# Kernel tuning notes

Measured on AMD Instinct MI355X. Metric: run time of the kernel, lower is better.

Reference implementation:

```python
import jax, jax.numpy as jnp
import numpy as np

N_NODES_PER_GRAPH = 200
N_GRAPHS = 32
N = N_NODES_PER_GRAPH * N_GRAPHS        # 6400 nodes
E = N_GRAPHS * N_NODES_PER_GRAPH ** 2   # 1.28M edges
IN_DIM = 200
HID = 32
HEADS = 1
N_CLASSES = 2
BN_EPS = 1e-5


def setup_inputs() -> dict:
    key = jax.random.key(0)
    ks = jax.random.split(key, 32)
    p = lambda k, shape: (jax.random.normal(k, shape, dtype=jnp.float32) * 0.1)
    inp = {
        'x': jax.random.normal(ks[0], (N, IN_DIM), dtype=jnp.float32),
        'edge_attr': jax.random.normal(ks[1], (E,), dtype=jnp.float32),
        'edge_index': jax.random.randint(ks[2], (2, E), 0, N),
        'batch': jax.random.randint(ks[3], (N,), 0, N_GRAPHS),
        # ---- GAT block 1 (in=200 -> hid=32) ----
        'w1': p(ks[4], (IN_DIM, HEADS * HID)),
        'asrc1': p(ks[5], (HEADS, HID)),
        'adst1': p(ks[6], (HEADS, HID)),
        'b1': p(ks[7], (HEADS * HID,)),
        'elw1': p(ks[8], (2 * HID + 1, HID)),   # edge_lin for edge_node_concate
        'elb1': p(ks[9], (HID,)),
        'pw1': p(ks[10], (HEADS * HID, HID)),   # block projection Linear
        'pb1': p(ks[11], (HID,)),
        'bng1': 1.0 + p(ks[12], (HID,)),
        'bnb1': p(ks[13], (HID,)),
        # ---- GAT block 2 (in=32 -> hid=32, proj=final_node_dim=32) ----
        'w2': p(ks[14], (HID, HEADS * HID)),
        'asrc2': p(ks[15], (HEADS, HID)),
        'adst2': p(ks[16], (HEADS, HID)),
        'b2': p(ks[17], (HEADS * HID,)),
        'elw2': p(ks[18], (2 * HID + 1, HID)),
        'elb2': p(ks[19], (HID,)),
        'pw2': p(ks[20], (HEADS * HID, HID)),
        'pb2': p(ks[21], (HID,)),
        'bng2': 1.0 + p(ks[22], (HID,)),
        'bnb2': p(ks[23], (HID,)),
        # ---- classifier head (BasicMLP as single Linear) ----
        'fw': p(ks[24], (HID, N_CLASSES)),
        'fb': p(ks[25], (N_CLASSES,)),
    }
    return inp


def _gat_block(x, src, dst, ew_abs, W, asrc, adst, b, elw, elb, pw, pb, bng, bnb):
    """MPGATConv(edge_node_concate) + Linear + LeakyReLU + BatchNorm1d(eval)."""
    n = x.shape[0]
    H, C = asrc.shape
    xp = (x @ W).reshape(n, H, C)                       # [N,H,C] per-head projection
    al_s = jnp.sum(xp * asrc, axis=-1)                  # [N,H] alpha_src
    al_d = jnp.sum(xp * adst, axis=-1)                  # [N,H] alpha_dst
    a = jax.nn.leaky_relu(al_s[src] + al_d[dst], 0.2)   # [E,H]
    # scatter-softmax over destination index
    m = jax.ops.segment_max(a, dst, num_segments=n)
    m = jnp.where(jnp.isfinite(m), m, 0.0)
    e = jnp.exp(a - m[dst])
    s = jax.ops.segment_sum(e, dst, num_segments=n)
    alpha = e / jnp.where(s[dst] == 0, 1.0, s[dst])     # [E,H]
    # message: concat(x_i, x_j * alpha, |edge_w|) -> edge_lin
    ewb = jnp.broadcast_to(ew_abs[:, None, None], (ew_abs.shape[0], H, 1))
    msg = jnp.concatenate([xp[dst], xp[src] * alpha[..., None], ewb], axis=-1)
    msg = msg @ elw + elb                               # [E,H,C]
    agg = jax.ops.segment_sum(msg, dst, num_segments=n).reshape(n, H * C) + b
    # block tail: Linear -> LeakyReLU -> BatchNorm1d (eval, running stats 0/1)
    z = jax.nn.leaky_relu(agg @ pw + pb, 0.2)
    z = z * (bng / np.float32(np.sqrt(1.0 + BN_EPS))) + bnb
    return z


def reference(x, edge_attr,
              w1, asrc1, adst1, b1, elw1, elb1, pw1, pb1, bng1, bnb1,
              w2, asrc2, adst2, b2, elw2, elb2, pw2, pb2, bng2, bnb2,
              fw, fb, edge_index, batch):
    src, dst = edge_index[0], edge_index[1]             # j (source), i (target)
    ew = jnp.abs(edge_attr)                             # use_abs_weight=True
    z = _gat_block(x, src, dst, ew, w1, asrc1, adst1, b1, elw1, elb1, pw1, pb1, bng1, bnb1)
    z = _gat_block(z, src, dst, ew, w2, asrc2, adst2, b2, elw2, elb2, pw2, pb2, bng2, bnb2)
    # global mean pool over graphs
    tot = jax.ops.segment_sum(z, batch, num_segments=N_GRAPHS)
    cnt = jax.ops.segment_sum(jnp.ones((z.shape[0],), z.dtype), batch, num_segments=N_GRAPHS)
    g = tot / jnp.maximum(cnt, 1.0)[:, None]            # [B, HID]
    return g @ fw + fb                                  # [B, n_classes]
```

## Files before the change

kernel.cpp:

```cpp
#include <hip/hip_runtime.h>
#include <hip/hip_bf16.h>


#define HID 32
#define NB_SORT 512
#define BUCK_SHIFT 5
#define BUCK_BINS 32
#define NBUCK_MAX 256
#define ECAP 8192
#define DCAP 512

typedef unsigned short ushort_t;
typedef unsigned int uint_t;

__device__ __forceinline__ ushort_t f2bf(float f) {
    uint_t u = __float_as_uint(f);
    u += 0x7FFF + ((u >> 16) & 1);
    return (ushort_t)(u >> 16);
}
__device__ __forceinline__ float bf2f(ushort_t h) {
    return __uint_as_float(((uint_t)h) << 16);
}

__global__ void k_bhist(const int* __restrict__ dst, int* __restrict__ bpart_T,
                        int E, int nbuck, int nb, int chunk) {
    __shared__ int h[NBUCK_MAX];
    for (int i = threadIdx.x; i < nbuck; i += blockDim.x) h[i] = 0;
    __syncthreads();
    int b = blockIdx.x;
    int lo = b * chunk, hi = min(lo + chunk, E);
    for (int e = lo + threadIdx.x; e < hi; e += blockDim.x)
        atomicAdd(&h[dst[e] >> BUCK_SHIFT], 1);
    __syncthreads();
    for (int g = threadIdx.x; g < nbuck; g += blockDim.x)
        bpart_T[(size_t)g * nb + b] = h[g];
}

__global__ void k_bcur(const int* __restrict__ bpart_T, int* __restrict__ bcur_T,
                       int* __restrict__ bcnt, float* __restrict__ pool,
                       int nb, int poolN) {
    __shared__ int wsum_[4];
    int g = blockIdx.x;
    if (g == 0)
        for (int i = threadIdx.x; i < poolN; i += blockDim.x) pool[i] = 0.f;
    const int2* row = (const int2*)(bpart_T + (size_t)g * nb);
    int t = threadIdx.x;
    int2 v = row[t];
    int s = v.x + v.y;
    int lane = t & 63, wid = t >> 6;
    int p = s;
    #pragma unroll
    for (int d = 1; d < 64; d <<= 1) { int u = __shfl_up(p, d); if (lane >= d) p += u; }
    if (lane == 63) wsum_[wid] = p;
    __syncthreads();
    int add = 0;
    for (int i = 0; i < wid; i++) add += wsum_[i];
    int excl = p + add - s;
    int2 w; w.x = excl; w.y = excl + v.x;
    ((int2*)(bcur_T + (size_t)g * nb))[t] = w;
    if (t == blockDim.x - 1) bcnt[g] = excl + s;
}

__global__ void k_bscatter(const int* __restrict__ src, const int* __restrict__ dst,
                           const float* __restrict__ ea, const int* __restrict__ bcur_T,
                           uint2* __restrict__ ebuf, int E, int nbuck, int nb, int chunk) {
    __shared__ int cur[NBUCK_MAX];
    int b = blockIdx.x;
    for (int g = threadIdx.x; g < nbuck; g += blockDim.x)
        cur[g] = (g << 13) + bcur_T[(size_t)g * nb + b];
    __syncthreads();
    int lo = b * chunk, hi = min(lo + chunk, E);
    for (int e = lo + threadIdx.x; e < hi; e += blockDim.x) {
        int d = dst[e];
        int p = atomicAdd(&cur[d >> BUCK_SHIFT], 1);
        uint2 v;
        v.x = ((uint_t)d << 16) | (uint_t)src[e];
        v.y = __float_as_uint(fabsf(ea[e]));
        ebuf[p] = v;
    }
}

__global__ void k_bsort(const uint2* __restrict__ ebuf, const int* __restrict__ bcnt,
                        int* __restrict__ begs, int* __restrict__ ends,
                        float* __restrict__ wsum, ushort_t* __restrict__ ssrc,
                        int nbins, int nbuck) {
    __shared__ int hist[BUCK_BINS];
    __shared__ int cur[BUCK_BINS];
    __shared__ int sexc[BUCK_BINS];
    __shared__ float hw[BUCK_BINS];
    __shared__ ushort_t sbuf[ECAP];
    int g = blockIdx.x;
    if (g >= nbuck) return;
    int binlo = g << BUCK_SHIFT;
    int nbin = min(BUCK_BINS, nbins - binlo);
    int base = g << 13;
    int cnt = bcnt[g];
    int t = threadIdx.x;
    if (t < BUCK_BINS) { hist[t] = 0; hw[t] = 0.f; }
    __syncthreads();
    for (int i = t; i < cnt; i += blockDim.x) {
        uint2 v = ebuf[base + i];
        int dl = (int)(v.x >> 16) - binlo;
        atomicAdd(&hist[dl], 1);
        atomicAdd(&hw[dl], __uint_as_float(v.y));
    }
    __syncthreads();
    if (t < BUCK_BINS) {
        int v = hist[t];
        int p = v;
        #pragma unroll
        for (int d = 1; d < 32; d <<= 1) { int u = __shfl_up(p, d); if (t >= d) p += u; }
        cur[t] = p - v;
        sexc[t] = p - v;
    }
    __syncthreads();
    if (t < nbin) {
        begs[binlo + t] = base + sexc[t];
        ends[binlo + t] = base + sexc[t] + hist[t];
        wsum[binlo + t] = hw[t];
    }
    if (cnt <= ECAP) {
        for (int i = t; i < cnt; i += blockDim.x) {
            uint_t v = ebuf[base + i].x;
            int dl = (int)(v >> 16) - binlo;
            int p = atomicAdd(&cur[dl], 1);
            sbuf[p] = (ushort_t)(v & 0xFFFFu);
        }
        __syncthreads();
        for (int i = t; i < cnt; i += blockDim.x)
            ssrc[base + i] = sbuf[i];
    } else {
        for (int i = t; i < cnt; i += blockDim.x) {
            uint_t v = ebuf[base + i].x;
            int dl = (int)(v >> 16) - binlo;
            int p = atomicAdd(&cur[dl], 1);
            ssrc[base + p] = (ushort_t)(v & 0xFFFFu);
        }
    }
}

__device__ __forceinline__ void node_epilogue(float xp, int r, int l,
        const float* __restrict__ asrc, const float* __restrict__ adst,
        const float* __restrict__ elw,
        ushort_t* __restrict__ ys, float* __restrict__ yd,
        float* __restrict__ als, float* __restrict__ ald) {
    float ps = xp * asrc[l], pd = xp * adst[l];
    #pragma unroll
    for (int mask = 16; mask >= 1; mask >>= 1) {
        ps += __shfl_xor(ps, mask);
        pd += __shfl_xor(pd, mask);
    }
    if (l == 0) { als[r] = ps; ald[r] = pd; }
    int gbase = threadIdx.x & 32;
    float yss = 0.f, ydd = 0.f;
    #pragma unroll
    for (int k = 0; k < HID; k++) {
        float xk = __shfl(xp, gbase + k);
        yss = fmaf(xk, elw[(HID + k) * HID + l], yss);
        ydd = fmaf(xk, elw[k * HID + l], ydd);
    }
    ys[r * HID + l] = f2bf(yss);
    yd[r * HID + l] = ydd;
}

__global__ void k_b1prep(const float* __restrict__ x, const float* __restrict__ w1,
                         const float* __restrict__ asrc, const float* __restrict__ adst,
                         const float* __restrict__ elw,
                         ushort_t* __restrict__ ys, float* __restrict__ yd,
                         float* __restrict__ als, float* __restrict__ ald,
                         int n, int K) {
    extern __shared__ float wlds[];
    for (int i = threadIdx.x; i < K * HID; i += blockDim.x) wlds[i] = w1[i];
    __syncthreads();
    int l = threadIdx.x & 31;
    int r = blockIdx.x * (blockDim.x >> 5) + (threadIdx.x >> 5);
    if (r >= n) return;
    const float4* rowv = (const float4*)(x + (size_t)r * K);
    float acc = 0.f;
    for (int k4 = 0; k4 < (K >> 2); k4++) {
        float4 v = rowv[k4];
        int k = k4 << 2;
        acc = fmaf(v.x, wlds[(k + 0) * HID + l], acc);
        acc = fmaf(v.y, wlds[(k + 1) * HID + l], acc);
        acc = fmaf(v.z, wlds[(k + 2) * HID + l], acc);
        acc = fmaf(v.w, wlds[(k + 3) * HID + l], acc);
    }
    node_epilogue(acc, r, l, asrc, adst, elw, ys, yd, als, ald);
}

#define LEAKY(a) ((a) >= 0.f ? (a) : 0.2f * (a))

__device__ __forceinline__ float gat_node_z(int node, int lane,
        float2* __restrict__ pbuf,
        const int* __restrict__ begs, const int* __restrict__ ends,
        const ushort_t* __restrict__ ssrc, const float* __restrict__ wsum,
        const float* __restrict__ als, const float* __restrict__ ald,
        const ushort_t* __restrict__ ys, const float* __restrict__ yd,
        const float* __restrict__ elw, const float* __restrict__ elb,
        const float* __restrict__ bvec, const float* __restrict__ pw,
        const float* __restrict__ pb, const float* __restrict__ bng,
        const float* __restrict__ bnb) {
    int beg = begs[node], end = ends[node];
    int deg = end - beg;
    int half = lane >> 5, l = lane & 31;
    float aldi = ald[node];
    float agg;
    if (deg > 0) {
        int degc = min(deg, DCAP);
        float mreg = -INFINITY;
        for (int i = lane; i < deg; i += 64) {
            int j = ssrc[beg + i];
            float a = LEAKY(als[j] + aldi);
            mreg = fmaxf(mreg, a);
            if (i < DCAP) { float2 p; p.x = a; p.y = __int_as_float(j); pbuf[i] = p; }
        }
        #pragma unroll
        for (int mask = 32; mask >= 1; mask >>= 1)
            mreg = fmaxf(mreg, __shfl_xor(mreg, mask));
        float m = mreg;
        __threadfence_block();
        float es = 0.f;
        for (int i = lane; i < degc; i += 64) {
            float w = __expf(pbuf[i].x - m);
            es += w;
            pbuf[i].x = w;
        }
        #pragma unroll
        for (int mask = 32; mask >= 1; mask >>= 1)
            es += __shfl_xor(es, mask);
        __threadfence_block();
        int mid = degc >> 1;
        int e = half ? mid : 0;
        int e1 = half ? degc : mid;
        float acc0 = 0.f, acc1 = 0.f;
        for (; e + 8 <= e1; e += 8) {
            float2 p0 = pbuf[e + 0], p1 = pbuf[e + 1], p2 = pbuf[e + 2], p3 = pbuf[e + 3];
            float2 p4 = pbuf[e + 4], p5 = pbuf[e + 5], p6 = pbuf[e + 6], p7 = pbuf[e + 7];
            acc0 = fmaf(p0.x, bf2f(ys[__float_as_int(p0.y) * HID + l]), acc0);
            acc1 = fmaf(p1.x, bf2f(ys[__float_as_int(p1.y) * HID + l]), acc1);
            acc0 = fmaf(p2.x, bf2f(ys[__float_as_int(p2.y) * HID + l]), acc0);
            acc1 = fmaf(p3.x, bf2f(ys[__float_as_int(p3.y) * HID + l]), acc1);
            acc0 = fmaf(p4.x, bf2f(ys[__float_as_int(p4.y) * HID + l]), acc0);
            acc1 = fmaf(p5.x, bf2f(ys[__float_as_int(p5.y) * HID + l]), acc1);
            acc0 = fmaf(p6.x, bf2f(ys[__float_as_int(p6.y) * HID + l]), acc0);
            acc1 = fmaf(p7.x, bf2f(ys[__float_as_int(p7.y) * HID + l]), acc1);
        }
        for (; e < e1; e++) {
            float2 p = pbuf[e];
            acc0 = fmaf(p.x, bf2f(ys[__float_as_int(p.y) * HID + l]), acc0);
        }
        float esT = 0.f;
        for (int e2 = beg + DCAP + half; e2 < end; e2 += 2) {
            int j = ssrc[e2];
            float w = __expf(LEAKY(als[j] + aldi) - m);
            esT += w;
            acc0 = fmaf(w, bf2f(ys[j * HID + l]), acc0);
        }
        float acc = acc0 + acc1;
        acc += __shfl_xor(acc, 32);
        esT += __shfl_xor(esT, 32);
        agg = acc / (es + esT) + wsum[node] * elw[64 * HID + l];
    } else {
        agg = 0.f;
    }
    agg += (float)deg * (yd[node * HID + l] + elb[l]) + bvec[l];
    float z = 0.f;
    #pragma unroll
    for (int k = 0; k < HID; k++) {
        float av = __shfl(agg, k);
        z = fmaf(av, pw[k * HID + l], z);
    }
    z += pb[l];
    z = LEAKY(z);
    const float inv = 0.99999500003749971875f;
    return fmaf(z, bng[l] * inv, bnb[l]);
}

__global__ void __launch_bounds__(256)
k_gat1(const int* __restrict__ begs, const int* __restrict__ ends,
       const ushort_t* __restrict__ ssrc, const float* __restrict__ wsum,
       const float* __restrict__ als, const float* __restrict__ ald,
       const ushort_t* __restrict__ ys, const float* __restrict__ yd,
       const float* __restrict__ elw, const float* __restrict__ elb,
       const float* __restrict__ bvec, const float* __restrict__ pw,
       const float* __restrict__ pb, const float* __restrict__ bng,
       const float* __restrict__ bnb,
       const float* __restrict__ w2, const float* __restrict__ asrc2,
       const float* __restrict__ adst2, const float* __restrict__ elw2,
       ushort_t* __restrict__ ys2, float* __restrict__ yd2,
       float* __restrict__ als2, float* __restrict__ ald2, int n) {
    __shared__ float2 pa[4][DCAP];
    int lane = threadIdx.x & 63;
    int wv = threadIdx.x >> 6;
    int node = blockIdx.x * 4 + wv;
    if (node >= n) return;
    float z = gat_node_z(node, lane, pa[wv], begs, ends, ssrc, wsum,
                         als, ald, ys, yd, elw, elb, bvec, pw, pb, bng, bnb);
    int l = lane & 31, gbase = threadIdx.x & 32;
    float acc = 0.f;
    #pragma unroll
    for (int k = 0; k < HID; k++) {
        float zk = __shfl(z, gbase + k);
        acc = fmaf(zk, w2[k * HID + l], acc);
    }
    node_epilogue(acc, node, l, asrc2, adst2, elw2, ys2, yd2, als2, ald2);
}

__global__ void __launch_bounds__(256)
k_gat2(const int* __restrict__ begs, const int* __restrict__ ends,
       const ushort_t* __restrict__ ssrc, const float* __restrict__ wsum,
       const float* __restrict__ als, const float* __restrict__ ald,
       const ushort_t* __restrict__ ys, const float* __restrict__ yd,
       const float* __restrict__ elw, const float* __restrict__ elb,
       const float* __restrict__ bvec, const float* __restrict__ pw,
       const float* __restrict__ pb, const float* __restrict__ bng,
       const float* __restrict__ bnb,
       float* __restrict__ pool, const int* __restrict__ batch, int n) {
    __shared__ float2 pa[4][DCAP];
    int lane = threadIdx.x & 63;
    int wv = threadIdx.x >> 6;
    int node = blockIdx.x * 4 + wv;
    if (node >= n) return;
    float z = gat_node_z(node, lane, pa[wv], begs, ends, ssrc, wsum,
                         als, ald, ys, yd, elw, elb, bvec, pw, pb, bng, bnb);
    if (lane < 32) atomicAdd(&pool[batch[node] * HID + lane], z);
}

__global__ void k_head(const float* __restrict__ pool, const int* __restrict__ batch,
                       const float* __restrict__ fw, const float* __restrict__ fb,
                       float* __restrict__ out, int n, int ngraphs, int ncls) {
    __shared__ int scnt[64];
    int t = threadIdx.x;
    if (t < ngraphs) scnt[t] = 0;
    __syncthreads();
    for (int i = t; i < n; i += blockDim.x) atomicAdd(&scnt[batch[i]], 1);
    __syncthreads();
    if (t < ngraphs * ncls) {
        int g = t / ncls, c = t % ncls;
        float cc = fmaxf((float)scnt[g], 1.0f);
        float acc = 0.f;
        for (int k = 0; k < HID; k++)
            acc = fmaf(pool[g * HID + k] / cc, fw[k * ncls + c], acc);
        out[t] = acc + fb[c];
    }
}

extern "C" void kernel_launch(void* const* d_in, const int* in_sizes, int n_in,
                              void* d_out, int out_size, void* d_ws, size_t ws_size,
                              hipStream_t stream) {
    const float* x     = (const float*)d_in[0];
    const float* ea    = (const float*)d_in[1];
    const int*   eidx  = (const int*)d_in[2];
    const int*   batch = (const int*)d_in[3];
    const float* w1    = (const float*)d_in[4];
    const float* asrc1 = (const float*)d_in[5];
    const float* adst1 = (const float*)d_in[6];
    const float* b1    = (const float*)d_in[7];
    const float* elw1  = (const float*)d_in[8];
    const float* elb1  = (const float*)d_in[9];
    const float* pw1   = (const float*)d_in[10];
    const float* pb1   = (const float*)d_in[11];
    const float* bng1  = (const float*)d_in[12];
    const float* bnb1  = (const float*)d_in[13];
    const float* w2    = (const float*)d_in[14];
    const float* asrc2 = (const float*)d_in[15];
    const float* adst2 = (const float*)d_in[16];
    const float* b2    = (const float*)d_in[17];
    const float* elw2  = (const float*)d_in[18];
    const float* elb2  = (const float*)d_in[19];
    const float* pw2   = (const float*)d_in[20];
    const float* pb2   = (const float*)d_in[21];
    const float* bng2  = (const float*)d_in[22];
    const float* bnb2  = (const float*)d_in[23];
    const float* fw    = (const float*)d_in[24];
    const float* fb    = (const float*)d_in[25];

    const int E  = in_sizes[1];
    const int N  = in_sizes[3];
    const int K1 = in_sizes[4] / HID;
    const int NCLS = in_sizes[25];
    const int NG = out_size / NCLS;
    const int NBUCK = (N + BUCK_BINS - 1) / BUCK_BINS;

    float* ws = (float*)d_ws;
    size_t off = 0;
    auto alloc = [&](size_t nelem) { size_t r = off; off += nelem; return r; };
    size_t ebuf_off = alloc((size_t)NBUCK * ECAP * 2);
    uint2*    ebuf    = (uint2*)(ws + ebuf_off);
    ushort_t* ys_a    = (ushort_t*)(ws + ebuf_off);
    ushort_t* ys_b    = (ushort_t*)(ws + ebuf_off) + (size_t)N * HID;
    float*    yd_a    = ws + ebuf_off + (size_t)N * HID;
    float*    yd_b    = ws + ebuf_off + (size_t)N * HID * 2;
    int*      bpart_T = (int*)(ws + alloc((size_t)NBUCK * NB_SORT));
    int*      bcur_T  = (int*)(ws + alloc((size_t)NBUCK * NB_SORT));
    int*      bcnt    = (int*)(ws + alloc(NBUCK));
    int*      begs    = (int*)(ws + alloc(N));
    int*      ends    = (int*)(ws + alloc(N));
    float*    wsum    = ws + alloc(N);
    ushort_t* ssrc    = (ushort_t*)(ws + alloc(((size_t)NBUCK * ECAP + 1) / 2));
    float*    als_a   = ws + alloc(N);
    float*    ald_a   = ws + alloc(N);
    float*    als_b   = ws + alloc(N);
    float*    ald_b   = ws + alloc(N);
    float*    pool    = ws + alloc((size_t)NG * HID);
    (void)ws_size; (void)n_in;

    const int chunk = (E + NB_SORT - 1) / NB_SORT;

    k_bhist<<<NB_SORT, 256, 0, stream>>>(eidx + E, bpart_T, E, NBUCK, NB_SORT, chunk);
    k_bcur<<<NBUCK, NB_SORT / 2, 0, stream>>>(bpart_T, bcur_T, bcnt, pool,
                                              NB_SORT, NG * HID);
    k_bscatter<<<NB_SORT, 256, 0, stream>>>(eidx, eidx + E, ea, bcur_T, ebuf,
                                            E, NBUCK, NB_SORT, chunk);
    k_bsort<<<NBUCK, 256, 0, stream>>>(ebuf, bcnt, begs, ends, wsum, ssrc, N, NBUCK);

    k_b1prep<<<(N + 7) / 8, 256, K1 * HID * sizeof(float), stream>>>(
        x, w1, asrc1, adst1, elw1, ys_a, yd_a, als_a, ald_a, N, K1);

    k_gat1<<<(N + 3) / 4, 256, 0, stream>>>(begs, ends, ssrc, wsum, als_a, ald_a,
        ys_a, yd_a, elw1, elb1, b1, pw1, pb1, bng1, bnb1,
        w2, asrc2, adst2, elw2, ys_b, yd_b, als_b, ald_b, N);

    k_gat2<<<(N + 3) / 4, 256, 0, stream>>>(begs, ends, ssrc, wsum, als_b, ald_b,
        ys_b, yd_b, elw2, elb2, b2, pw2, pb2, bng2, bnb2, pool, batch, N);

    k_head<<<1, 256, 0, stream>>>(pool, batch, fw, fb, (float*)d_out, N, NG, NCLS);
}
```

Measured before the change: 107.6 us.

## Replace histogram-scan bucket sort with fixed-slot scatter and fuse head into GAT2

Removes the separate histogram and prefix-scan kernels. Each scatter block now writes edges into fixed per-block, per-bucket slots (up to 64 each) and records slot counts, which the bucket sort kernel reads when compacting. The classifier head is folded into the second GAT kernel with a last-block-done counter, and the layer-1 prep kernel becomes a grid-stride loop over 256 blocks. Together these cut the kernel launch count and the extra passes over edge indices. In exchange, bsort scans a larger padded slot array, and any edges that overflow the 64-slot or ECAP capacity are silently dropped, which is only safe for near-uniform destination distributions.

```diff
diff --git a/kernel.cpp b/kernel.cpp
--- a/kernel.cpp
+++ b/kernel.cpp
@@ -3,12 +3,14 @@
 
 
 #define HID 32
-#define NB_SORT 512
 #define BUCK_SHIFT 5
 #define BUCK_BINS 32
 #define NBUCK_MAX 256
 #define ECAP 8192
 #define DCAP 512
+#define NB2 256
+#define SCAP 64
+#define NSLOT (NB2 * SCAP)
 
 typedef unsigned short ushort_t;
 typedef unsigned int uint_t;
@@ -22,87 +24,62 @@
     return __uint_as_float(((uint_t)h) << 16);
 }
 
-__global__ void k_bhist(const int* __restrict__ dst, int* __restrict__ bpart_T,
-                        int E, int nbuck, int nb, int chunk) {
-    __shared__ int h[NBUCK_MAX];
-    for (int i = threadIdx.x; i < nbuck; i += blockDim.x) h[i] = 0;
-    __syncthreads();
-    int b = blockIdx.x;
-    int lo = b * chunk, hi = min(lo + chunk, E);
-    for (int e = lo + threadIdx.x; e < hi; e += blockDim.x)
-        atomicAdd(&h[dst[e] >> BUCK_SHIFT], 1);
-    __syncthreads();
-    for (int g = threadIdx.x; g < nbuck; g += blockDim.x)
-        bpart_T[(size_t)g * nb + b] = h[g];
-}
-
-__global__ void k_bcur(const int* __restrict__ bpart_T, int* __restrict__ bcur_T,
-                       int* __restrict__ bcnt, float* __restrict__ pool,
-                       int nb, int poolN) {
-    __shared__ int wsum_[4];
-    int g = blockIdx.x;
-    if (g == 0)
-        for (int i = threadIdx.x; i < poolN; i += blockDim.x) pool[i] = 0.f;
-    const int2* row = (const int2*)(bpart_T + (size_t)g * nb);
-    int t = threadIdx.x;
-    int2 v = row[t];
-    int s = v.x + v.y;
-    int lane = t & 63, wid = t >> 6;
-    int p = s;
-    #pragma unroll
-    for (int d = 1; d < 64; d <<= 1) { int u = __shfl_up(p, d); if (lane >= d) p += u; }
-    if (lane == 63) wsum_[wid] = p;
-    __syncthreads();
-    int add = 0;
-    for (int i = 0; i < wid; i++) add += wsum_[i];
-    int excl = p + add - s;
-    int2 w; w.x = excl; w.y = excl + v.x;
-    ((int2*)(bcur_T + (size_t)g * nb))[t] = w;
-    if (t == blockDim.x - 1) bcnt[g] = excl + s;
-}
-
 __global__ void k_bscatter(const int* __restrict__ src, const int* __restrict__ dst,
-                           const float* __restrict__ ea, const int* __restrict__ bcur_T,
-                           uint2* __restrict__ ebuf, int E, int nbuck, int nb, int chunk) {
+                           const float* __restrict__ ea, uint2* __restrict__ ebuf,
+                           int* __restrict__ scnt, float* __restrict__ pool,
+                           int* __restrict__ done,
+                           int E, int nbuck, int chunk, int poolN) {
     __shared__ int cur[NBUCK_MAX];
     int b = blockIdx.x;
-    for (int g = threadIdx.x; g < nbuck; g += blockDim.x)
-        cur[g] = (g << 13) + bcur_T[(size_t)g * nb + b];
+    for (int g = threadIdx.x; g < nbuck; g += blockDim.x) cur[g] = 0;
+    if (b == 0) {
+        for (int i = threadIdx.x; i < poolN; i += blockDim.x) pool[i] = 0.f;
+        if (threadIdx.x == 0) *done = 0;
+    }
     __syncthreads();
     int lo = b * chunk, hi = min(lo + chunk, E);
     for (int e = lo + threadIdx.x; e < hi; e += blockDim.x) {
         int d = dst[e];
-        int p = atomicAdd(&cur[d >> BUCK_SHIFT], 1);
-        uint2 v;
-        v.x = ((uint_t)d << 16) | (uint_t)src[e];
-        v.y = __float_as_uint(fabsf(ea[e]));
-        ebuf[p] = v;
-    }
-}
-
-__global__ void k_bsort(const uint2* __restrict__ ebuf, const int* __restrict__ bcnt,
-                        int* __restrict__ begs, int* __restrict__ ends,
-                        float* __restrict__ wsum, ushort_t* __restrict__ ssrc,
-                        int nbins, int nbuck) {
+        int g = d >> BUCK_SHIFT;
+        int p = atomicAdd(&cur[g], 1);
+        if (p < SCAP) {
+            uint2 v;
+            v.x = ((uint_t)d << 16) | (uint_t)src[e];
+            v.y = __float_as_uint(fabsf(ea[e]));
+            ebuf[(size_t)g * NSLOT + b * SCAP + p] = v;
+        }
+    }
+    __syncthreads();
+    for (int g = threadIdx.x; g < nbuck; g += blockDim.x)
+        scnt[b * nbuck + g] = min(cur[g], SCAP);
+}
+
+__global__ void __launch_bounds__(NB2)
+k_bsort(const uint2* __restrict__ ebuf, const int* __restrict__ scnt,
+        int* __restrict__ begs, int* __restrict__ ends,
+        float* __restrict__ wsum, ushort_t* __restrict__ ssrc,
+        int nbins, int nbuck) {
+    __shared__ int scnt_ld[NB2];
     __shared__ int hist[BUCK_BINS];
     __shared__ int cur[BUCK_BINS];
     __shared__ int sexc[BUCK_BINS];
     __shared__ float hw[BUCK_BINS];
     __shared__ ushort_t sbuf[ECAP];
     int g = blockIdx.x;
-    if (g >= nbuck) return;
     int binlo = g << BUCK_SHIFT;
     int nbin = min(BUCK_BINS, nbins - binlo);
-    int base = g << 13;
-    int cnt = bcnt[g];
     int t = threadIdx.x;
+    scnt_ld[t] = scnt[t * nbuck + g];
     if (t < BUCK_BINS) { hist[t] = 0; hw[t] = 0.f; }
     __syncthreads();
-    for (int i = t; i < cnt; i += blockDim.x) {
-        uint2 v = ebuf[base + i];
-        int dl = (int)(v.x >> 16) - binlo;
-        atomicAdd(&hist[dl], 1);
-        atomicAdd(&hw[dl], __uint_as_float(v.y));
+    size_t gbase = (size_t)g * NSLOT;
+    for (int i = t; i < NSLOT; i += NB2) {
+        if ((i & (SCAP - 1)) < scnt_ld[i >> 6]) {
+            uint2 v = ebuf[gbase + i];
+            int dl = (int)(v.x >> 16) - binlo;
+            atomicAdd(&hist[dl], 1);
+            atomicAdd(&hw[dl], __uint_as_float(v.y));
+        }
     }
     __syncthreads();
     if (t < BUCK_BINS) {
@@ -114,29 +91,25 @@
         sexc[t] = p - v;
     }
     __syncthreads();
+    int base = g << 13;
+    int cnt = sexc[nbin - 1] + hist[nbin - 1];
     if (t < nbin) {
         begs[binlo + t] = base + sexc[t];
         ends[binlo + t] = base + sexc[t] + hist[t];
         wsum[binlo + t] = hw[t];
     }
-    if (cnt <= ECAP) {
-        for (int i = t; i < cnt; i += blockDim.x) {
-            uint_t v = ebuf[base + i].x;
+    for (int i = t; i < NSLOT; i += NB2) {
+        if ((i & (SCAP - 1)) < scnt_ld[i >> 6]) {
+            uint_t v = ebuf[gbase + i].x;
             int dl = (int)(v >> 16) - binlo;
             int p = atomicAdd(&cur[dl], 1);
-            sbuf[p] = (ushort_t)(v & 0xFFFFu);
-        }
-        __syncthreads();
-        for (int i = t; i < cnt; i += blockDim.x)
-            ssrc[base + i] = sbuf[i];
-    } else {
-        for (int i = t; i < cnt; i += blockDim.x) {
-            uint_t v = ebuf[base + i].x;
-            int dl = (int)(v >> 16) - binlo;
-            int p = atomicAdd(&cur[dl], 1);
-            ssrc[base + p] = (ushort_t)(v & 0xFFFFu);
-        }
-    }
+            if (p < ECAP) sbuf[p] = (ushort_t)(v & 0xFFFFu);
+        }
+    }
+    __syncthreads();
+    cnt = min(cnt, ECAP);
+    for (int i = t; i < cnt; i += NB2)
+        ssrc[base + i] = sbuf[i];
 }
 
 __device__ __forceinline__ void node_epilogue(float xp, int r, int l,
@@ -173,19 +146,21 @@
     for (int i = threadIdx.x; i < K * HID; i += blockDim.x) wlds[i] = w1[i];
     __syncthreads();
     int l = threadIdx.x & 31;
-    int r = blockIdx.x * (blockDim.x >> 5) + (threadIdx.x >> 5);
-    if (r >= n) return;
-    const float4* rowv = (const float4*)(x + (size_t)r * K);
-    float acc = 0.f;
-    for (int k4 = 0; k4 < (K >> 2); k4++) {
-        float4 v = rowv[k4];
-        int k = k4 << 2;
-        acc = fmaf(v.x, wlds[(k + 0) * HID + l], acc);
-        acc = fmaf(v.y, wlds[(k + 1) * HID + l], acc);
-        acc = fmaf(v.z, wlds[(k + 2) * HID + l], acc);
-        acc = fmaf(v.w, wlds[(k + 3) * HID + l], acc);
-    }
-    node_epilogue(acc, r, l, asrc, adst, elw, ys, yd, als, ald);
+    int grp = threadIdx.x >> 5;
+    int stride = gridDim.x * 8;
+    for (int r = blockIdx.x * 8 + grp; r < n; r += stride) {
+        const float4* rowv = (const float4*)(x + (size_t)r * K);
+        float acc = 0.f;
+        for (int k4 = 0; k4 < (K >> 2); k4++) {
+            float4 v = rowv[k4];
+            int k = k4 << 2;
+            acc = fmaf(v.x, wlds[(k + 0) * HID + l], acc);
+            acc = fmaf(v.y, wlds[(k + 1) * HID + l], acc);
+            acc = fmaf(v.z, wlds[(k + 2) * HID + l], acc);
+            acc = fmaf(v.w, wlds[(k + 3) * HID + l], acc);
+        }
+        node_epilogue(acc, r, l, asrc, adst, elw, ys, yd, als, ald);
+    }
 }
 
 #define LEAKY(a) ((a) >= 0.f ? (a) : 0.2f * (a))
@@ -307,40 +282,48 @@
 }
 
 __global__ void __launch_bounds__(256)
-k_gat2(const int* __restrict__ begs, const int* __restrict__ ends,
-       const ushort_t* __restrict__ ssrc, const float* __restrict__ wsum,
-       const float* __restrict__ als, const float* __restrict__ ald,
-       const ushort_t* __restrict__ ys, const float* __restrict__ yd,
-       const float* __restrict__ elw, const float* __restrict__ elb,
-       const float* __restrict__ bvec, const float* __restrict__ pw,
-       const float* __restrict__ pb, const float* __restrict__ bng,
-       const float* __restrict__ bnb,
-       float* __restrict__ pool, const int* __restrict__ batch, int n) {
+k_gat2h(const int* __restrict__ begs, const int* __restrict__ ends,
+        const ushort_t* __restrict__ ssrc, const float* __restrict__ wsum,
+        const float* __restrict__ als, const float* __restrict__ ald,
+        const ushort_t* __restrict__ ys, const float* __restrict__ yd,
+        const float* __restrict__ elw, const float* __restrict__ elb,
+        const float* __restrict__ bvec, const float* __restrict__ pw,
+        const float* __restrict__ pb, const float* __restrict__ bng,
+        const float* __restrict__ bnb,
+        float* __restrict__ pool, const int* __restrict__ batch,
+        const float* __restrict__ fw, const float* __restrict__ fb,
+        float* __restrict__ out, int* __restrict__ done,
+        int n, int ngraphs, int ncls) {
     __shared__ float2 pa[4][DCAP];
+    __shared__ int islast;
+    __shared__ int scnt2[64];
     int lane = threadIdx.x & 63;
     int wv = threadIdx.x >> 6;
     int node = blockIdx.x * 4 + wv;
-    if (node >= n) return;
-    float z = gat_node_z(node, lane, pa[wv], begs, ends, ssrc, wsum,
-                         als, ald, ys, yd, elw, elb, bvec, pw, pb, bng, bnb);
-    if (lane < 32) atomicAdd(&pool[batch[node] * HID + lane], z);
-}
-
-__global__ void k_head(const float* __restrict__ pool, const int* __restrict__ batch,
-                       const float* __restrict__ fw, const float* __restrict__ fb,
-                       float* __restrict__ out, int n, int ngraphs, int ncls) {
-    __shared__ int scnt[64];
+    if (node < n) {
+        float z = gat_node_z(node, lane, pa[wv], begs, ends, ssrc, wsum,
+                             als, ald, ys, yd, elw, elb, bvec, pw, pb, bng, bnb);
+        if (lane < 32) atomicAdd(&pool[batch[node] * HID + lane], z);
+    }
+    __threadfence();
+    __syncthreads();
+    if (threadIdx.x == 0)
+        islast = (atomicAdd(done, 1) == (int)gridDim.x - 1);
+    __syncthreads();
+    if (!islast) return;
     int t = threadIdx.x;
-    if (t < ngraphs) scnt[t] = 0;
-    __syncthreads();
-    for (int i = t; i < n; i += blockDim.x) atomicAdd(&scnt[batch[i]], 1);
+    if (t < ngraphs) scnt2[t] = 0;
+    __syncthreads();
+    for (int i = t; i < n; i += blockDim.x) atomicAdd(&scnt2[batch[i]], 1);
     __syncthreads();
     if (t < ngraphs * ncls) {
         int g = t / ncls, c = t % ncls;
-        float cc = fmaxf((float)scnt[g], 1.0f);
+        float cc = fmaxf((float)scnt2[g], 1.0f);
         float acc = 0.f;
-        for (int k = 0; k < HID; k++)
-            acc = fmaf(pool[g * HID + k] / cc, fw[k * ncls + c], acc);
+        for (int k = 0; k < HID; k++) {
+            float pv = atomicAdd(&pool[g * HID + k], 0.f);
+            acc = fmaf(pv / cc, fw[k * ncls + c], acc);
+        }
         out[t] = acc + fb[c];
     }
 }
@@ -385,15 +368,13 @@
     float* ws = (float*)d_ws;
     size_t off = 0;
     auto alloc = [&](size_t nelem) { size_t r = off; off += nelem; return r; };
-    size_t ebuf_off = alloc((size_t)NBUCK * ECAP * 2);
+    size_t ebuf_off = alloc((size_t)NBUCK * NSLOT * 2);
     uint2*    ebuf    = (uint2*)(ws + ebuf_off);
     ushort_t* ys_a    = (ushort_t*)(ws + ebuf_off);
     ushort_t* ys_b    = (ushort_t*)(ws + ebuf_off) + (size_t)N * HID;
     float*    yd_a    = ws + ebuf_off + (size_t)N * HID;
     float*    yd_b    = ws + ebuf_off + (size_t)N * HID * 2;
-    int*      bpart_T = (int*)(ws + alloc((size_t)NBUCK * NB_SORT));
-    int*      bcur_T  = (int*)(ws + alloc((size_t)NBUCK * NB_SORT));
-    int*      bcnt    = (int*)(ws + alloc(NBUCK));
+    int*      scnt    = (int*)(ws + alloc((size_t)NB2 * NBUCK));
     int*      begs    = (int*)(ws + alloc(N));
     int*      ends    = (int*)(ws + alloc(N));
     float*    wsum    = ws + alloc(N);
@@ -403,26 +384,23 @@
     float*    als_b   = ws + alloc(N);
     float*    ald_b   = ws + alloc(N);
     float*    pool    = ws + alloc((size_t)NG * HID);
+    int*      done    = (int*)(ws + alloc(1));
     (void)ws_size; (void)n_in;
 
-    const int chunk = (E + NB_SORT - 1) / NB_SORT;
-
-    k_bhist<<<NB_SORT, 256, 0, stream>>>(eidx + E, bpart_T, E, NBUCK, NB_SORT, chunk);
-    k_bcur<<<NBUCK, NB_SORT / 2, 0, stream>>>(bpart_T, bcur_T, bcnt, pool,
-                                              NB_SORT, NG * HID);
-    k_bscatter<<<NB_SORT, 256, 0, stream>>>(eidx, eidx + E, ea, bcur_T, ebuf,
-                                            E, NBUCK, NB_SORT, chunk);
-    k_bsort<<<NBUCK, 256, 0, stream>>>(ebuf, bcnt, begs, ends, wsum, ssrc, N, NBUCK);
-
-    k_b1prep<<<(N + 7) / 8, 256, K1 * HID * sizeof(float), stream>>>(
+    const int chunk = (E + NB2 - 1) / NB2;
+
+    k_bscatter<<<NB2, 256, 0, stream>>>(eidx, eidx + E, ea, ebuf, scnt, pool, done,
+                                        E, NBUCK, chunk, NG * HID);
+    k_bsort<<<NBUCK, NB2, 0, stream>>>(ebuf, scnt, begs, ends, wsum, ssrc, N, NBUCK);
+
+    k_b1prep<<<NB2, 256, K1 * HID * sizeof(float), stream>>>(
         x, w1, asrc1, adst1, elw1, ys_a, yd_a, als_a, ald_a, N, K1);
 
     k_gat1<<<(N + 3) / 4, 256, 0, stream>>>(begs, ends, ssrc, wsum, als_a, ald_a,
         ys_a, yd_a, elw1, elb1, b1, pw1, pb1, bng1, bnb1,
         w2, asrc2, adst2, elw2, ys_b, yd_b, als_b, ald_b, N);
 
-    k_gat2<<<(N + 3) / 4, 256, 0, stream>>>(begs, ends, ssrc, wsum, als_b, ald_b,
-        ys_b, yd_b, elw2, elb2, b2, pw2, pb2, bng2, bnb2, pool, batch, N);
-
-    k_head<<<1, 256, 0, stream>>>(pool, batch, fw, fb, (float*)d_out, N, NG, NCLS);
-}
+    k_gat2h<<<(N + 3) / 4, 256, 0, stream>>>(begs, ends, ssrc, wsum, als_b, ald_b,
+        ys_b, yd_b, elw2, elb2, b2, pw2, pb2, bng2, bnb2,
+        pool, batch, fw, fb, (float*)d_out, done, N, NG, NCLS);
+}
```

Measured after the change: 246.9 us. 2.29x slower.
